# Performance work log

Measured on AMD Instinct MI355X. Metric: run time of the kernel, lower is better.

Reference implementation:

```python
import jax, jax.numpy as jnp
import numpy as np
import math

B, L, D, H, FF = 4, 1024, 1024, 16, 4096
DH = D // H
EPS = 1e-12


def layer_norm(x, gamma, beta):
    mean = x.mean(-1, keepdims=True)
    var = ((x - mean) ** 2).mean(-1, keepdims=True)  # biased var, matches unbiased=False
    return gamma * (x - mean) / jnp.sqrt(var + EPS) + beta


def setup_inputs() -> dict:
    key = jax.random.key(0)
    ks = jax.random.split(key, 16)
    s = 0.02
    return {
        "x": jax.random.normal(ks[0], (B, L, D), jnp.float32),
        "attn_bias": jax.random.uniform(ks[1], (B, L, L), jnp.float32),
        "src_mask": jax.random.randint(ks[2], (B, L), 0, 2, jnp.int32),
        "wq": jax.random.normal(ks[3], (D, D), jnp.float32) * s,
        "bq": jnp.zeros((D,), jnp.float32),
        "wk": jax.random.normal(ks[4], (D, D), jnp.float32) * s,
        "bk": jnp.zeros((D,), jnp.float32),
        "wv": jax.random.normal(ks[5], (D, D), jnp.float32) * s,
        "bv": jnp.zeros((D,), jnp.float32),
        "wo": jax.random.normal(ks[6], (D, D), jnp.float32) * s,
        "bo": jnp.zeros((D,), jnp.float32),
        "gamma1": jnp.ones((D,), jnp.float32),
        "beta1": jnp.zeros((D,), jnp.float32),
        "w1": jax.random.normal(ks[7], (D, FF), jnp.float32) * s,
        "b1": jnp.zeros((FF,), jnp.float32),
        "w2": jax.random.normal(ks[8], (FF, D), jnp.float32) * s,
        "b2": jnp.zeros((D,), jnp.float32),
        "gamma2": jnp.ones((D,), jnp.float32),
        "beta2": jnp.zeros((D,), jnp.float32),
    }


def reference(x, attn_bias, src_mask, wq, bq, wk, bk, wv, bv, wo, bo,
              gamma1, beta1, w1, b1, w2, b2, gamma2, beta2):
    # ---- multi-head attention with multiplicative bias + additive mask ----
    def split_heads(t):  # [B,L,D] -> [B,H,L,DH]
        return t.reshape(B, L, H, DH).transpose(0, 2, 1, 3)

    q = split_heads(x @ wq + bq)
    k = split_heads(x @ wk + bk)
    v = split_heads(x @ wv + bv)

    score = jnp.einsum('bhqd,bhkd->bhqk', q, k) / math.sqrt(DH)
    score = score * attn_bias[:, None, :, :]               # multiplicative bias
    score = jnp.where(src_mask[:, None, None, :] == 0, -10000.0, score)
    p = jax.nn.softmax(score, axis=-1)
    ctx = jnp.einsum('bhqk,bhkd->bhqd', p, v)
    ctx = ctx.transpose(0, 2, 1, 3).reshape(B, L, D)
    attn_out = ctx @ wo + bo

    h = layer_norm(x + attn_out, gamma1, beta1)

    # ---- position-wise FFN ----
    ffn = jax.nn.relu(h @ w1 + b1) @ w2 + b2
    out = layer_norm(h + ffn, gamma2, beta2)
    return out
```

## Files before the change

### kernel.cpp

```cpp
#include <hip/hip_runtime.h>
#include <hip/hip_bf16.h>
#include <math.h>

#define BB 4
#define LL 1024
#define DD 1024
#define HH 16
#define DHH 64
#define FFF 4096
#define MM (BB*LL)
#define LDQ 3072

typedef __attribute__((ext_vector_type(8))) short short8;
typedef __attribute__((ext_vector_type(4))) float f32x4;

__device__ __forceinline__ ushort f2bf(float f) {
    __hip_bfloat16 h = __float2bfloat16(f);
    return *(ushort*)&h;
}
__device__ __forceinline__ float bf2f(ushort u) {
    __hip_bfloat16 h = *(__hip_bfloat16*)&u;
    return __bfloat162float(h);
}
__device__ __forceinline__ float fexp2(float x) {
#if __has_builtin(__builtin_amdgcn_exp2f)
    return __builtin_amdgcn_exp2f(x);
#else
    return exp2f(x);
#endif
}

__device__ __forceinline__ float block_reduce_sum(float v, float* red, int tid) {
    red[tid] = v;
    __syncthreads();
    for (int off = 128; off > 0; off >>= 1) {
        if (tid < off) red[tid] += red[tid + off];
        __syncthreads();
    }
    float r = red[0];
    __syncthreads();
    return r;
}

__global__ __launch_bounds__(256)
void cast_bf16(const float* __restrict__ in, ushort* __restrict__ out) {
    const int i = blockIdx.x * 256 + threadIdx.x;
    float4 v = ((const float4*)in)[i];
    ushort4 o;
    o.x = f2bf(v.x); o.y = f2bf(v.y); o.z = f2bf(v.z); o.w = f2bf(v.w);
    ((ushort4*)out)[i] = o;
}

__global__ __launch_bounds__(256)
void swizzle_bias(const float* __restrict__ bias, float* __restrict__ B) {
    __shared__ float rowbuf[1024];
    const int row = blockIdx.x;
    const int t = threadIdx.x;
    *(float4*)&rowbuf[t * 4] = *(const float4*)&bias[(size_t)row * 1024 + t * 4];
    __syncthreads();
    const int kt = t >> 4, c = t & 15;
    const float s = 1.4426950408889634f;
    float4 o;
    o.x = rowbuf[kt * 64 + 0 * 16 + c] * s;
    o.y = rowbuf[kt * 64 + 1 * 16 + c] * s;
    o.z = rowbuf[kt * 64 + 2 * 16 + c] * s;
    o.w = rowbuf[kt * 64 + 3 * 16 + c] * s;
    *(float4*)&B[(size_t)row * 1024 + t * 4] = o;
}

__global__ __launch_bounds__(256)
void transpose_cast(const float* __restrict__ W, ushort* __restrict__ WT,
                    int K, int N) {
    __shared__ float tile[32][33];
    const int n0 = blockIdx.x * 32, k0 = blockIdx.y * 32;
    const int t = threadIdx.x;
    const int r = t >> 3, c4 = (t & 7) * 4;
    float4 v = *(const float4*)&W[(size_t)(k0 + r) * N + n0 + c4];
    tile[r][c4 + 0] = v.x; tile[r][c4 + 1] = v.y;
    tile[r][c4 + 2] = v.z; tile[r][c4 + 3] = v.w;
    __syncthreads();
    ushort4 o;
    o.x = f2bf(tile[c4 + 0][r]);
    o.y = f2bf(tile[c4 + 1][r]);
    o.z = f2bf(tile[c4 + 2][r]);
    o.w = f2bf(tile[c4 + 3][r]);
    *(ushort4*)&WT[(size_t)(n0 + r) * K + k0 + c4] = o;
}

__global__ __launch_bounds__(256)
void concat3(const float* __restrict__ a, const float* __restrict__ b,
             const float* __restrict__ c, float* __restrict__ o) {
    const int i = blockIdx.x * 256 + threadIdx.x;
    o[i] = (i < 1024) ? a[i] : ((i < 2048) ? b[i - 1024] : c[i - 2048]);
}

template<int BN>
__global__ __launch_bounds__(256)
void gemm_bf16(const ushort* __restrict__ A, const ushort* __restrict__ Bt,
               const float* __restrict__ bias, void* __restrict__ C,
               ushort* __restrict__ Vt, int vn0,
               int M, int N, int K, int relu, int obf16, int qlim) {
    constexpr int JF = BN / 32;
    __shared__ ushort Als0[128 * 32];
    __shared__ ushort Als1[128 * 32];
    __shared__ ushort Bls0[BN * 32];
    __shared__ ushort Bls1[BN * 32];

    const int L = blockIdx.x + gridDim.x * blockIdx.y;
    const int xcd = L & 7;
    const int idx = L >> 3;
    const int mpx = gridDim.y >> 3;
    const int bm = (xcd * mpx + (idx % mpx)) * 128;
    const int bn = (idx / mpx) * BN;

    const int t = threadIdx.x;
    const int lane = t & 63;
    const int w = t >> 6;
    const int wm = (w >> 1) * 64;
    const int wn = (w & 1) * (BN / 2);
    const int fm = lane & 15;
    const int kg = lane >> 4;

    f32x4 acc[4][JF] = {};

    for (int k0 = 0; k0 < K; k0 += 64) {
        #pragma unroll
        for (int j = 0; j < 2; ++j) {
            const int chunk = j * 256 + t;
            const int row = chunk >> 2, kc = chunk & 3;
            const ushort* ga0 = A + (size_t)(bm + row) * K + k0 + kc * 8;
            __builtin_amdgcn_global_load_lds(
                (const __attribute__((address_space(1))) void*)ga0,
                (__attribute__((address_space(3))) void*)(Als0 + chunk * 8), 16, 0, 0);
            const ushort* ga1 = ga0 + 32;
            __builtin_amdgcn_global_load_lds(
                (const __attribute__((address_space(1))) void*)ga1,
                (__attribute__((address_space(3))) void*)(Als1 + chunk * 8), 16, 0, 0);
        }
        #pragma unroll
        for (int j = 0; j < BN / 64; ++j) {
            const int chunk = j * 256 + t;
            const int row = chunk >> 2, kc = chunk & 3;
            const ushort* gb0 = Bt + (size_t)(bn + row) * K + k0 + kc * 8;
            __builtin_amdgcn_global_load_lds(
                (const __attribute__((address_space(1))) void*)gb0,
                (__attribute__((address_space(3))) void*)(Bls0 + chunk * 8), 16, 0, 0);
            const ushort* gb1 = gb0 + 32;
            __builtin_amdgcn_global_load_lds(
                (const __attribute__((address_space(1))) void*)gb1,
                (__attribute__((address_space(3))) void*)(Bls1 + chunk * 8), 16, 0, 0);
        }
        __syncthreads();

        short8 af[4][2], bfr[JF][2];
        #pragma unroll
        for (int i = 0; i < 4; ++i) {
            af[i][0] = *(const short8*)&Als0[(wm + i * 16 + fm) * 32 + kg * 8];
            af[i][1] = *(const short8*)&Als1[(wm + i * 16 + fm) * 32 + kg * 8];
        }
        #pragma unroll
        for (int j = 0; j < JF; ++j) {
            bfr[j][0] = *(const short8*)&Bls0[(wn + j * 16 + fm) * 32 + kg * 8];
            bfr[j][1] = *(const short8*)&Bls1[(wn + j * 16 + fm) * 32 + kg * 8];
        }
        #pragma unroll
        for (int i = 0; i < 4; ++i)
            #pragma unroll
            for (int j = 0; j < JF; ++j) {
                acc[i][j] = __builtin_amdgcn_mfma_f32_16x16x32_bf16(
                    af[i][0], bfr[j][0], acc[i][j], 0, 0, 0);
                acc[i][j] = __builtin_amdgcn_mfma_f32_16x16x32_bf16(
                    af[i][1], bfr[j][1], acc[i][j], 0, 0, 0);
            }
        __syncthreads();
    }

    const int orow0 = (lane >> 4) * 4;
    const int ocol = lane & 15;
    #pragma unroll
    for (int j = 0; j < JF; ++j) {
        const int n = bn + wn + j * 16 + ocol;
        const float bv = bias[n];
        const bool isV = (bn + wn + j * 16) >= vn0;
        #pragma unroll
        for (int i = 0; i < 4; ++i) {
            const int m0 = bm + wm + i * 16 + orow0;
            if (isV) {
                ushort4 o;
                float v0 = acc[i][j][0] + bv, v1 = acc[i][j][1] + bv;
                float v2 = acc[i][j][2] + bv, v3 = acc[i][j][3] + bv;
                o.x = f2bf(v0); o.y = f2bf(v1); o.z = f2bf(v2); o.w = f2bf(v3);
                *(ushort4*)&Vt[((size_t)((m0 >> 10) << 10) + (n - vn0)) * 1024 + (m0 & 1023)] = o;
            } else {
                #pragma unroll
                for (int r = 0; r < 4; ++r) {
                    const int m = m0 + r;
                    float v = acc[i][j][r] + bv;
                    if (relu) v = fmaxf(v, 0.0f);
                    if (n < qlim) v *= 0.125f;
                    if (obf16)
                        ((ushort*)C)[(size_t)m * N + n] = f2bf(v);
                    else
                        ((float*)C)[(size_t)m * N + n] = v;
                }
            }
        }
    }
}

template<int BN>
__global__ __launch_bounds__(256)
void gemm_bf16_sk(const ushort* __restrict__ A, const ushort* __restrict__ Bt,
                  float* __restrict__ P, int M, int N, int K) {
    constexpr int JF = BN / 32;
    __shared__ ushort Als0[128 * 32];
    __shared__ ushort Als1[128 * 32];
    __shared__ ushort Bls0[BN * 32];
    __shared__ ushort Bls1[BN * 32];

    const int L = blockIdx.x + gridDim.x * blockIdx.y;
    const int xcd = L & 7;
    const int idx = L >> 3;
    const int mpx = gridDim.y >> 3;
    const int bm = (xcd * mpx + (idx % mpx)) * 128;
    const int bn = (idx / mpx) * BN;
    const int kbeg = blockIdx.z * (K >> 1);
    const int kend = kbeg + (K >> 1);

    const int t = threadIdx.x;
    const int lane = t & 63;
    const int w = t >> 6;
    const int wm = (w >> 1) * 64;
    const int wn = (w & 1) * (BN / 2);
    const int fm = lane & 15;
    const int kg = lane >> 4;

    f32x4 acc[4][JF] = {};

    for (int k0 = kbeg; k0 < kend; k0 += 64) {
        #pragma unroll
        for (int j = 0; j < 2; ++j) {
            const int chunk = j * 256 + t;
            const int row = chunk >> 2, kc = chunk & 3;
            const ushort* ga0 = A + (size_t)(bm + row) * K + k0 + kc * 8;
            __builtin_amdgcn_global_load_lds(
                (const __attribute__((address_space(1))) void*)ga0,
                (__attribute__((address_space(3))) void*)(Als0 + chunk * 8), 16, 0, 0);
            const ushort* ga1 = ga0 + 32;
            __builtin_amdgcn_global_load_lds(
                (const __attribute__((address_space(1))) void*)ga1,
                (__attribute__((address_space(3))) void*)(Als1 + chunk * 8), 16, 0, 0);
        }
        #pragma unroll
        for (int j = 0; j < BN / 64; ++j) {
            const int chunk = j * 256 + t;
            const int row = chunk >> 2, kc = chunk & 3;
            const ushort* gb0 = Bt + (size_t)(bn + row) * K + k0 + kc * 8;
            __builtin_amdgcn_global_load_lds(
                (const __attribute__((address_space(1))) void*)gb0,
                (__attribute__((address_space(3))) void*)(Bls0 + chunk * 8), 16, 0, 0);
            const ushort* gb1 = gb0 + 32;
            __builtin_amdgcn_global_load_lds(
                (const __attribute__((address_space(1))) void*)gb1,
                (__attribute__((address_space(3))) void*)(Bls1 + chunk * 8), 16, 0, 0);
        }
        __syncthreads();

        short8 af[4][2], bfr[JF][2];
        #pragma unroll
        for (int i = 0; i < 4; ++i) {
            af[i][0] = *(const short8*)&Als0[(wm + i * 16 + fm) * 32 + kg * 8];
            af[i][1] = *(const short8*)&Als1[(wm + i * 16 + fm) * 32 + kg * 8];
        }
        #pragma unroll
        for (int j = 0; j < JF; ++j) {
            bfr[j][0] = *(const short8*)&Bls0[(wn + j * 16 + fm) * 32 + kg * 8];
            bfr[j][1] = *(const short8*)&Bls1[(wn + j * 16 + fm) * 32 + kg * 8];
        }
        #pragma unroll
        for (int i = 0; i < 4; ++i)
            #pragma unroll
            for (int j = 0; j < JF; ++j) {
                acc[i][j] = __builtin_amdgcn_mfma_f32_16x16x32_bf16(
                    af[i][0], bfr[j][0], acc[i][j], 0, 0, 0);
                acc[i][j] = __builtin_amdgcn_mfma_f32_16x16x32_bf16(
                    af[i][1], bfr[j][1], acc[i][j], 0, 0, 0);
            }
        __syncthreads();
    }

    float* Pz = P + (size_t)blockIdx.z * M * N;
    const int orow0 = (lane >> 4) * 4;
    const int ocol = lane & 15;
    #pragma unroll
    for (int j = 0; j < JF; ++j) {
        const int n = bn + wn + j * 16 + ocol;
        #pragma unroll
        for (int i = 0; i < 4; ++i) {
            const int m0 = bm + wm + i * 16 + orow0;
            #pragma unroll
            for (int r = 0; r < 4; ++r)
                Pz[(size_t)(m0 + r) * N + n] = acc[i][j][r];
        }
    }
}


#define BARM() asm volatile("s_barrier" ::: "memory")
#define VMC4() asm volatile("s_waitcnt vmcnt(4)" ::: "memory")
#define LGK0() do { asm volatile("s_waitcnt lgkmcnt(0)" ::: "memory"); \
                    __builtin_amdgcn_sched_barrier(0); } while (0)

__device__ __forceinline__ short8 fragrd(const ushort* h, int row, int s, int kg) {
    const int cb = ((s << 6) + (kg << 4)) ^ (((row >> 2) & 1) << 5);
    return *(const short8*)(h + row * 64 + (cb >> 1));
}

__device__ __forceinline__ void stage_half(const ushort* __restrict__ src,
                                           int srcK, ushort* ldsh, int t) {
    #pragma unroll
    for (int l = 0; l < 2; ++l) {
        const int chunk = l * 512 + t;
        const int r = chunk >> 3;
        const int cb_log = ((chunk & 7) * 16) ^ (((r >> 2) & 1) << 5);
        const ushort* g = src + (size_t)r * srcK + (cb_log >> 1);
        __builtin_amdgcn_global_load_lds(
            (const __attribute__((address_space(1))) void*)g,
            (__attribute__((address_space(3))) void*)(ldsh + chunk * 8), 16, 0, 0);
    }
}

__global__ __launch_bounds__(512, 2)
void gemm256(const ushort* __restrict__ A, const ushort* __restrict__ Bt,
             const float* __restrict__ bias, ushort* __restrict__ C,
             int M, int N, int K, int relu) {
    __shared__ ushort lds[65536];

    const int nt = K >> 6;
    const int t = threadIdx.x;
    const int lane = t & 63;
    const int w = t >> 6;
    const int wr = w >> 2, wc = w & 3;
    const int fm = lane & 15, kg = lane >> 4;

    const int bid = blockIdx.x;
    const int wg = (bid & 7) * (gridDim.x >> 3) + (bid >> 3);
    const int bm = (wg & 15) << 8;
    const int bn = (wg >> 4) << 8;

    ushort* const A0 = lds;
    ushort* const B0 = lds + 16384;
    ushort* const A1 = lds + 32768;
    ushort* const B1 = lds + 49152;

    const ushort* const Ah0 = A0 + wr * 8192;
    const ushort* const Ah1 = A1 + wr * 8192;
    const ushort* const Bh0 = B0 + (wc >> 1) * 8192;
    const ushort* const Bh1 = B1 + (wc >> 1) * 8192;
    const int brow = (wc & 1) * 64;

    #define ASRC(tt, h) (A  + (size_t)(bm + (h) * 128) * K + (tt) * 64)
    #define BSRC(tt, h) (Bt + (size_t)(bn + (h) * 128) * K + (tt) * 64)

    f32x4 acc[8][4] = {};
    short8 af[4][2];
    short8 bf2[4][2];

    #define RD_A(HP, MI0) do { \
        _Pragma("unroll") \
        for (int i = 0; i < 4; ++i) { \
            const int row = ((MI0) + i) * 16 + fm; \
            af[i][0] = fragrd((HP), row, 0, kg); \
            af[i][1] = fragrd((HP), row, 1, kg); \
        } } while (0)

    #define RD_B(HP, J0) do { \
        _Pragma("unroll") \
        for (int jj = 0; jj < 2; ++jj) { \
            const int row = brow + ((J0) + jj) * 16 + fm; \
            bf2[(J0) + jj][0] = fragrd((HP), row, 0, kg); \
            bf2[(J0) + jj][1] = fragrd((HP), row, 1, kg); \
        } } while (0)

    #define QMFMA(MI0, J0) do { \
        __builtin_amdgcn_s_setprio(1); \
        _Pragma("unroll") \
        for (int i = 0; i < 4; ++i) { \
            _Pragma("unroll") \
            for (int jj = 0; jj < 2; ++jj) { \
                acc[(MI0)+i][(J0)+jj] = __builtin_amdgcn_mfma_f32_16x16x32_bf16( \
                    af[i][0], bf2[(J0)+jj][0], acc[(MI0)+i][(J0)+jj], 0, 0, 0); \
                acc[(MI0)+i][(J0)+jj] = __builtin_amdgcn_mfma_f32_16x16x32_bf16( \
                    af[i][1], bf2[(J0)+jj][1], acc[(MI0)+i][(J0)+jj], 0, 0, 0); \
            } } \
        __builtin_amdgcn_s_setprio(0); \
    } while (0)

    stage_half(BSRC(0, 0), K, B0, t);
    stage_half(BSRC(0, 1), K, B0 + 8192, t);
    stage_half(ASRC(0, 0), K, A0, t);
    stage_half(ASRC(0, 1), K, A0 + 8192, t);
    stage_half(BSRC(1, 0), K, B1, t);
    stage_half(BSRC(1, 1), K, B1 + 8192, t);
    VMC4();
    BARM();

    for (int it = 0; it < (nt >> 1); ++it) {
        const int ta = 2 * it;
        const int tb = ta + 1;
        const int t2 = min(ta + 2, nt - 1);
        const int t3 = min(ta + 3, nt - 1);

        RD_A(Ah0, 0); RD_B(Bh0, 0);
        stage_half(ASRC(tb, 0), K, A1, t);
        BARM(); LGK0(); QMFMA(0, 0); BARM();
        RD_B(Bh0, 2);
        stage_half(ASRC(tb, 1), K, A1 + 8192, t);
        BARM(); LGK0(); QMFMA(0, 2); BARM();
        RD_A(Ah0, 4);
        stage_half(BSRC(t2, 0), K, B0, t);
        BARM(); LGK0(); QMFMA(4, 2); BARM();
        stage_half(BSRC(t2, 1), K, B0 + 8192, t);
        VMC4();
        BARM(); LGK0(); QMFMA(4, 0); BARM();
        RD_A(Ah1, 0); RD_B(Bh1, 0);
        stage_half(ASRC(t2, 0), K, A0, t);
        BARM(); LGK0(); QMFMA(0, 0); BARM();
        RD_B(Bh1, 2);
        stage_half(ASRC(t2, 1), K, A0 + 8192, t);
        BARM(); LGK0(); QMFMA(0, 2); BARM();
        RD_A(Ah1, 4);
        stage_half(BSRC(t3, 0), K, B1, t);
        BARM(); LGK0(); QMFMA(4, 2); BARM();
        stage_half(BSRC(t3, 1), K, B1 + 8192, t);
        VMC4();
        BARM(); LGK0(); QMFMA(4, 0); BARM();
    }

    const int oc = lane & 15, og = lane >> 4;
    #pragma unroll
    for (int nj = 0; nj < 4; ++nj) {
        const int n = bn + wc * 64 + nj * 16 + oc;
        const float bv = bias[n];
        #pragma unroll
        for (int mi = 0; mi < 8; ++mi) {
            const int m0 = bm + wr * 128 + mi * 16 + og * 4;
            #pragma unroll
            for (int r = 0; r < 4; ++r) {
                float v = acc[mi][nj][r] + bv;
                if (relu) v = fmaxf(v, 0.0f);
                C[(size_t)(m0 + r) * N + n] = f2bf(v);
            }
        }
    }
    #undef ASRC
    #undef BSRC
    #undef RD_A
    #undef RD_B
    #undef QMFMA
}

__global__ __launch_bounds__(256, 4)
void attn_mfma(const ushort* __restrict__ QKVb, const ushort* __restrict__ Vt,
               const float* __restrict__ biasw, const int* __restrict__ mask,
               ushort* __restrict__ ctx) {
    const int q0 = blockIdx.x * 64;
    const int h = blockIdx.y;
    const int b = blockIdx.z;
    const int t = threadIdx.x;
    const int lane = t & 63;
    const int w = t >> 6;
    const int g = lane >> 4;
    const int c = lane & 15;

    __shared__ ushort QP[64 * 72];
    __shared__ ushort Ks[64 * 72];
    __shared__ ushort Vs[64 * 72];
    __shared__ float maskS[LL];

    #pragma unroll
    for (int i = 0; i < 2; ++i) {
        const int chunk = i * 256 + t;
        const int row = chunk >> 3, c8 = (chunk & 7) * 8;
        *(short8*)&QP[row * 72 + c8] =
            *(const short8*)(QKVb + ((size_t)(b * LL + q0 + row)) * LDQ + h * DHH + c8);
    }
    {
        int4 mi = ((const int4*)(mask + b * LL))[t];
        float4 mf;
        mf.x = mi.x ? 0.0f : -49152.0f;
        mf.y = mi.y ? 0.0f : -49152.0f;
        mf.z = mi.z ? 0.0f : -49152.0f;
        mf.w = mi.w ? 0.0f : -49152.0f;
        ((float4*)maskS)[t] = mf;
    }

    short8 pk[2], pv[2];
    #pragma unroll
    for (int i = 0; i < 2; ++i) {
        const int chunk = i * 256 + t;
        const int row = chunk >> 3, c8 = (chunk & 7) * 8;
        pk[i] = *(const short8*)(QKVb + ((size_t)(b * LL + row)) * LDQ + 1024 + h * DHH + c8);
        pv[i] = *(const short8*)(Vt + ((size_t)((b * HH + h) * DHH + row)) * LL + c8);
    }
    __syncthreads();

    short8 aq0 = *(const short8*)&QP[(w * 16 + c) * 72 + g * 8];
    short8 aq1 = *(const short8*)&QP[(w * 16 + c) * 72 + g * 8 + 32];
    ushort* Pw = QP + w * (16 * 72);

    const float* bp = biasw + (size_t)(b * LL + q0 + w * 16 + 4 * g) * 1024 + c * 4;
    float4 pb[4];
    #pragma unroll
    for (int r = 0; r < 4; ++r)
        pb[r] = *(const float4*)(bp + r * 1024);

    float l_run[4] = {0.f, 0.f, 0.f, 0.f};
    f32x4 acc_o[4] = {};

    for (int kt = 0; kt < 16; ++kt) {
        #pragma unroll
        for (int i = 0; i < 2; ++i) {
            const int chunk = i * 256 + t;
            const int row = chunk >> 3, c8 = (chunk & 7) * 8;
            *(short8*)&Ks[row * 72 + c8] = pk[i];
            *(short8*)&Vs[row * 72 + c8] = pv[i];
        }
        __syncthreads();

        if (kt < 15) {
            const int k0n = (kt + 1) * 64;
            #pragma unroll
            for (int i = 0; i < 2; ++i) {
                const int chunk = i * 256 + t;
                const int row = chunk >> 3, c8 = (chunk & 7) * 8;
                pk[i] = *(const short8*)(QKVb + ((size_t)(b * LL + k0n + row)) * LDQ + 1024 + h * DHH + c8);
                pv[i] = *(const short8*)(Vt + ((size_t)((b * HH + h) * DHH + row)) * LL + k0n + c8);
            }
        }

        float4 pbn[4];
        if (kt < 15) {
            #pragma unroll
            for (int r = 0; r < 4; ++r)
                pbn[r] = *(const float4*)(bp + r * 1024 + (kt + 1) * 64);
        }

        float mk[4];
        #pragma unroll
        for (int j = 0; j < 4; ++j) mk[j] = maskS[kt * 64 + j * 16 + c];

        f32x4 accs[4] = {};
        __builtin_amdgcn_s_setprio(1);
        #pragma unroll
        for (int j = 0; j < 4; ++j) {
            short8 bk0 = *(const short8*)&Ks[(j * 16 + c) * 72 + g * 8];
            short8 bk1 = *(const short8*)&Ks[(j * 16 + c) * 72 + g * 8 + 32];
            accs[j] = __builtin_amdgcn_mfma_f32_16x16x32_bf16(aq0, bk0, accs[j], 0, 0, 0);
            accs[j] = __builtin_amdgcn_mfma_f32_16x16x32_bf16(aq1, bk1, accs[j], 0, 0, 0);
        }
        __builtin_amdgcn_s_setprio(0);

        #pragma unroll
        for (int j = 0; j < 4; ++j)
            #pragma unroll
            for (int r = 0; r < 4; ++r) {
                const float pe = fexp2(fmaf(accs[j][r], ((const float*)&pb[r])[j], mk[j]));
                l_run[r] += pe;
                Pw[(4 * g + r) * 72 + j * 16 + c] = f2bf(pe);
            }

        __builtin_amdgcn_s_setprio(1);
        #pragma unroll
        for (int ks = 0; ks < 2; ++ks) {
            short8 ap = *(const short8*)&Pw[c * 72 + ks * 32 + g * 8];
            #pragma unroll
            for (int j = 0; j < 4; ++j) {
                short8 bv8 = *(const short8*)&Vs[(j * 16 + c) * 72 + ks * 32 + g * 8];
                acc_o[j] = __builtin_amdgcn_mfma_f32_16x16x32_bf16(ap, bv8, acc_o[j], 0, 0, 0);
            }
        }
        __builtin_amdgcn_s_setprio(0);

        if (kt < 15) {
            #pragma unroll
            for (int r = 0; r < 4; ++r) pb[r] = pbn[r];
        }
        __syncthreads();
    }

    #pragma unroll
    for (int r = 0; r < 4; ++r) {
        float l = l_run[r];
        #pragma unroll
        for (int d = 1; d < 16; d <<= 1) l += __shfl_xor(l, d);
        const float inv = 1.0f / l;
        #pragma unroll
        for (int j = 0; j < 4; ++j)
            ctx[((size_t)(b * LL + q0 + w * 16 + 4 * g + r)) * DD + h * DHH + j * 16 + c] =
                f2bf(acc_o[j][r] * inv);
    }
}

__global__ __launch_bounds__(256)
void add_ln_kernel(const float* __restrict__ P0, const float* __restrict__ P1,
                   const float* __restrict__ cb, const float* __restrict__ bres,
                   const float* __restrict__ gamma, const float* __restrict__ beta,
                   float* __restrict__ out, ushort* __restrict__ outb) {
    const int row = blockIdx.x;
    const int tid = threadIdx.x;
    __shared__ float red[256];

    const size_t base = (size_t)row * DD;
    float v[4];
    float sum = 0.0f;
    #pragma unroll
    for (int i = 0; i < 4; ++i) {
        const int col = tid + i * 256;
        v[i] = P0[base + col] + P1[base + col] + cb[col] + bres[base + col];
        sum += v[i];
    }
    const float mean = block_reduce_sum(sum, red, tid) * (1.0f / 1024.0f);
    float vs = 0.0f;
    #pragma unroll
    for (int i = 0; i < 4; ++i) {
        const float dlt = v[i] - mean;
        vs += dlt * dlt;
    }
    const float var = block_reduce_sum(vs, red, tid) * (1.0f / 1024.0f);
    const float rstd = rsqrtf(var + 1e-12f);
    #pragma unroll
    for (int i = 0; i < 4; ++i) {
        const int col = tid + i * 256;
        const float o = gamma[col] * (v[i] - mean) * rstd + beta[col];
        out[base + col] = o;
        if (outb) outb[base + col] = f2bf(o);
    }
}

extern "C" void kernel_launch(void* const* d_in, const int* in_sizes, int n_in,
                              void* d_out, int out_size, void* d_ws, size_t ws_size,
                              hipStream_t stream) {
    const float* x         = (const float*)d_in[0];
    const float* attn_bias = (const float*)d_in[1];
    const int*   src_mask  = (const int*)  d_in[2];
    const float* wq = (const float*)d_in[3];
    const float* bq = (const float*)d_in[4];
    const float* wk = (const float*)d_in[5];
    const float* bk = (const float*)d_in[6];
    const float* wv = (const float*)d_in[7];
    const float* bv = (const float*)d_in[8];
    const float* wo = (const float*)d_in[9];
    const float* bo = (const float*)d_in[10];
    const float* gamma1 = (const float*)d_in[11];
    const float* beta1  = (const float*)d_in[12];
    const float* w1 = (const float*)d_in[13];
    const float* b1 = (const float*)d_in[14];
    const float* w2 = (const float*)d_in[15];
    const float* b2 = (const float*)d_in[16];
    const float* gamma2 = (const float*)d_in[17];
    const float* beta2  = (const float*)d_in[18];
    float* out = (float*)d_out;

    const size_t MB = 1024 * 1024;
    char* W = (char*)d_ws;
    ushort* xb    = (ushort*)(W + 0);
    ushort* ctxb  = (ushort*)(W + 0);
    ushort* W1T   = (ushort*)(W + 0);
    ushort* QKVb  = (ushort*)(W + 8 * MB);
    float*  Hb    = (float*) (W + 8 * MB);
    ushort* Hbb   = (ushort*)(W + 24 * MB);
    ushort* W2T   = (ushort*)(W + 24 * MB);
    ushort* F1b   = (ushort*)(W + 32 * MB);
    ushort* Vt    = (ushort*)(W + 40 * MB);
    ushort* WQKVT = (ushort*)(W + 48 * MB);
    ushort* WOT   = (ushort*)(W + 48 * MB);
    float*  bqkv  = (float*) (W + 62 * MB);
    float*  biasw = (float*) (W + 64 * MB);
    float*  P0    = (float*) (W + 64 * MB);

    dim3 blk(256);

    cast_bf16<<<dim3(4096), blk, 0, stream>>>(x, xb);
    swizzle_bias<<<dim3(4096), blk, 0, stream>>>(attn_bias, biasw);
    transpose_cast<<<dim3(32, 32), blk, 0, stream>>>(wq, WQKVT, DD, DD);
    transpose_cast<<<dim3(32, 32), blk, 0, stream>>>(wk, WQKVT + 1024 * 1024, DD, DD);
    transpose_cast<<<dim3(32, 32), blk, 0, stream>>>(wv, WQKVT + 2048 * 1024, DD, DD);
    concat3<<<dim3(12), blk, 0, stream>>>(bq, bk, bv, bqkv);
    gemm_bf16<128><<<dim3(24, 32), blk, 0, stream>>>(xb, WQKVT, bqkv, QKVb,
                                                     Vt, 2048, MM, LDQ, DD, 0, 1, 1024);
    attn_mfma<<<dim3(16, HH, BB), blk, 0, stream>>>(QKVb, Vt, biasw, src_mask, ctxb);
    transpose_cast<<<dim3(32, 32), blk, 0, stream>>>(wo, WOT, DD, DD);
    gemm_bf16_sk<64><<<dim3(16, 32, 2), blk, 0, stream>>>(ctxb, WOT, P0, MM, DD, DD);
    transpose_cast<<<dim3(128, 32), blk, 0, stream>>>(w1, W1T, DD, FFF);
    add_ln_kernel<<<dim3(MM), blk, 0, stream>>>(P0, P0 + (size_t)MM * DD, bo, x,
                                                gamma1, beta1, Hb, Hbb);
    gemm256<<<dim3(256), dim3(512), 0, stream>>>(Hbb, W1T, b1, F1b, MM, FFF, DD, 1);
    transpose_cast<<<dim3(32, 128), blk, 0, stream>>>(w2, W2T, FFF, DD);
    gemm_bf16_sk<64><<<dim3(16, 32, 2), blk, 0, stream>>>(F1b, W2T, P0, MM, DD, FFF);
    add_ln_kernel<<<dim3(MM), blk, 0, stream>>>(P0, P0 + (size_t)MM * DD, b2, Hb,
                                                gamma2, beta2, out, nullptr);
}
```

Baseline: 374.6 us.

## Run QKV projection through 256x256 gemm256 kernel and widen LDS swizzle

The fused QKV projection now uses the larger 256x256-tile gemm256 kernel instead of the 128x128 gemm_bf16, which is removed. gemm256's epilogue gains the V-transpose write and Q scaling so it can produce the QKV outputs. The LDS XOR swizzle changes from a single-bit pattern to an eight-way (row & 7) pattern to cut bank conflicts on fragment reads. The larger tiles raise data reuse but launch only 192 workgroups, which may leave some compute units idle.

```diff
diff --git a/kernel.cpp b/kernel.cpp
--- a/kernel.cpp
+++ b/kernel.cpp
@@ -96,10 +96,8 @@
 
 template<int BN>
 __global__ __launch_bounds__(256)
-void gemm_bf16(const ushort* __restrict__ A, const ushort* __restrict__ Bt,
-               const float* __restrict__ bias, void* __restrict__ C,
-               ushort* __restrict__ Vt, int vn0,
-               int M, int N, int K, int relu, int obf16, int qlim) {
+void gemm_bf16_sk(const ushort* __restrict__ A, const ushort* __restrict__ Bt,
+                  float* __restrict__ P, int M, int N, int K) {
     constexpr int JF = BN / 32;
     __shared__ ushort Als0[128 * 32];
     __shared__ ushort Als1[128 * 32];
@@ -112,6 +110,8 @@
     const int mpx = gridDim.y >> 3;
     const int bm = (xcd * mpx + (idx % mpx)) * 128;
     const int bn = (idx / mpx) * BN;
+    const int kbeg = blockIdx.z * (K >> 1);
+    const int kend = kbeg + (K >> 1);
 
     const int t = threadIdx.x;
     const int lane = t & 63;
@@ -123,7 +123,7 @@
 
     f32x4 acc[4][JF] = {};
 
-    for (int k0 = 0; k0 < K; k0 += 64) {
+    for (int k0 = kbeg; k0 < kend; k0 += 64) {
         #pragma unroll
         for (int j = 0; j < 2; ++j) {
             const int chunk = j * 256 + t;
@@ -175,120 +175,6 @@
         __syncthreads();
     }
 
-    const int orow0 = (lane >> 4) * 4;
-    const int ocol = lane & 15;
-    #pragma unroll
-    for (int j = 0; j < JF; ++j) {
-        const int n = bn + wn + j * 16 + ocol;
-        const float bv = bias[n];
-        const bool isV = (bn + wn + j * 16) >= vn0;
-        #pragma unroll
-        for (int i = 0; i < 4; ++i) {
-            const int m0 = bm + wm + i * 16 + orow0;
-            if (isV) {
-                ushort4 o;
-                float v0 = acc[i][j][0] + bv, v1 = acc[i][j][1] + bv;
-                float v2 = acc[i][j][2] + bv, v3 = acc[i][j][3] + bv;
-                o.x = f2bf(v0); o.y = f2bf(v1); o.z = f2bf(v2); o.w = f2bf(v3);
-                *(ushort4*)&Vt[((size_t)((m0 >> 10) << 10) + (n - vn0)) * 1024 + (m0 & 1023)] = o;
-            } else {
-                #pragma unroll
-                for (int r = 0; r < 4; ++r) {
-                    const int m = m0 + r;
-                    float v = acc[i][j][r] + bv;
-                    if (relu) v = fmaxf(v, 0.0f);
-                    if (n < qlim) v *= 0.125f;
-                    if (obf16)
-                        ((ushort*)C)[(size_t)m * N + n] = f2bf(v);
-                    else
-                        ((float*)C)[(size_t)m * N + n] = v;
-                }
-            }
-        }
-    }
-}
-
-template<int BN>
-__global__ __launch_bounds__(256)
-void gemm_bf16_sk(const ushort* __restrict__ A, const ushort* __restrict__ Bt,
-                  float* __restrict__ P, int M, int N, int K) {
-    constexpr int JF = BN / 32;
-    __shared__ ushort Als0[128 * 32];
-    __shared__ ushort Als1[128 * 32];
-    __shared__ ushort Bls0[BN * 32];
-    __shared__ ushort Bls1[BN * 32];
-
-    const int L = blockIdx.x + gridDim.x * blockIdx.y;
-    const int xcd = L & 7;
-    const int idx = L >> 3;
-    const int mpx = gridDim.y >> 3;
-    const int bm = (xcd * mpx + (idx % mpx)) * 128;
-    const int bn = (idx / mpx) * BN;
-    const int kbeg = blockIdx.z * (K >> 1);
-    const int kend = kbeg + (K >> 1);
-
-    const int t = threadIdx.x;
-    const int lane = t & 63;
-    const int w = t >> 6;
-    const int wm = (w >> 1) * 64;
-    const int wn = (w & 1) * (BN / 2);
-    const int fm = lane & 15;
-    const int kg = lane >> 4;
-
-    f32x4 acc[4][JF] = {};
-
-    for (int k0 = kbeg; k0 < kend; k0 += 64) {
-        #pragma unroll
-        for (int j = 0; j < 2; ++j) {
-            const int chunk = j * 256 + t;
-            const int row = chunk >> 2, kc = chunk & 3;
-            const ushort* ga0 = A + (size_t)(bm + row) * K + k0 + kc * 8;
-            __builtin_amdgcn_global_load_lds(
-                (const __attribute__((address_space(1))) void*)ga0,
-                (__attribute__((address_space(3))) void*)(Als0 + chunk * 8), 16, 0, 0);
-            const ushort* ga1 = ga0 + 32;
-            __builtin_amdgcn_global_load_lds(
-                (const __attribute__((address_space(1))) void*)ga1,
-                (__attribute__((address_space(3))) void*)(Als1 + chunk * 8), 16, 0, 0);
-        }
-        #pragma unroll
-        for (int j = 0; j < BN / 64; ++j) {
-            const int chunk = j * 256 + t;
-            const int row = chunk >> 2, kc = chunk & 3;
-            const ushort* gb0 = Bt + (size_t)(bn + row) * K + k0 + kc * 8;
-            __builtin_amdgcn_global_load_lds(
-                (const __attribute__((address_space(1))) void*)gb0,
-                (__attribute__((address_space(3))) void*)(Bls0 + chunk * 8), 16, 0, 0);
-            const ushort* gb1 = gb0 + 32;
-            __builtin_amdgcn_global_load_lds(
-                (const __attribute__((address_space(1))) void*)gb1,
-                (__attribute__((address_space(3))) void*)(Bls1 + chunk * 8), 16, 0, 0);
-        }
-        __syncthreads();
-
-        short8 af[4][2], bfr[JF][2];
-        #pragma unroll
-        for (int i = 0; i < 4; ++i) {
-            af[i][0] = *(const short8*)&Als0[(wm + i * 16 + fm) * 32 + kg * 8];
-            af[i][1] = *(const short8*)&Als1[(wm + i * 16 + fm) * 32 + kg * 8];
-        }
-        #pragma unroll
-        for (int j = 0; j < JF; ++j) {
-            bfr[j][0] = *(const short8*)&Bls0[(wn + j * 16 + fm) * 32 + kg * 8];
-            bfr[j][1] = *(const short8*)&Bls1[(wn + j * 16 + fm) * 32 + kg * 8];
-        }
-        #pragma unroll
-        for (int i = 0; i < 4; ++i)
-            #pragma unroll
-            for (int j = 0; j < JF; ++j) {
-                acc[i][j] = __builtin_amdgcn_mfma_f32_16x16x32_bf16(
-                    af[i][0], bfr[j][0], acc[i][j], 0, 0, 0);
-                acc[i][j] = __builtin_amdgcn_mfma_f32_16x16x32_bf16(
-                    af[i][1], bfr[j][1], acc[i][j], 0, 0, 0);
-            }
-        __syncthreads();
-    }
-
     float* Pz = P + (size_t)blockIdx.z * M * N;
     const int orow0 = (lane >> 4) * 4;
     const int ocol = lane & 15;
@@ -312,7 +198,7 @@
                     __builtin_amdgcn_sched_barrier(0); } while (0)
 
 __device__ __forceinline__ short8 fragrd(const ushort* h, int row, int s, int kg) {
-    const int cb = ((s << 6) + (kg << 4)) ^ (((row >> 2) & 1) << 5);
+    const int cb = ((s << 6) + (kg << 4)) ^ ((row & 7) << 4);
     return *(const short8*)(h + row * 64 + (cb >> 1));
 }
 
@@ -322,7 +208,7 @@
     for (int l = 0; l < 2; ++l) {
         const int chunk = l * 512 + t;
         const int r = chunk >> 3;
-        const int cb_log = ((chunk & 7) * 16) ^ (((r >> 2) & 1) << 5);
+        const int cb_log = ((chunk & 7) * 16) ^ ((r & 7) << 4);
         const ushort* g = src + (size_t)r * srcK + (cb_log >> 1);
         __builtin_amdgcn_global_load_lds(
             (const __attribute__((address_space(1))) void*)g,
@@ -333,7 +219,8 @@
 __global__ __launch_bounds__(512, 2)
 void gemm256(const ushort* __restrict__ A, const ushort* __restrict__ Bt,
              const float* __restrict__ bias, ushort* __restrict__ C,
-             int M, int N, int K, int relu) {
+             ushort* __restrict__ Vt, int vn0,
+             int M, int N, int K, int relu, int qlim) {
     __shared__ ushort lds[65536];
 
     const int nt = K >> 6;
@@ -440,16 +327,28 @@
     const int oc = lane & 15, og = lane >> 4;
     #pragma unroll
     for (int nj = 0; nj < 4; ++nj) {
-        const int n = bn + wc * 64 + nj * 16 + oc;
+        const int nb = bn + wc * 64 + nj * 16;
+        const int n = nb + oc;
         const float bv = bias[n];
+        const bool isV = nb >= vn0;
         #pragma unroll
         for (int mi = 0; mi < 8; ++mi) {
             const int m0 = bm + wr * 128 + mi * 16 + og * 4;
-            #pragma unroll
-            for (int r = 0; r < 4; ++r) {
-                float v = acc[mi][nj][r] + bv;
-                if (relu) v = fmaxf(v, 0.0f);
-                C[(size_t)(m0 + r) * N + n] = f2bf(v);
+            if (isV) {
+                ushort4 o;
+                o.x = f2bf(acc[mi][nj][0] + bv);
+                o.y = f2bf(acc[mi][nj][1] + bv);
+                o.z = f2bf(acc[mi][nj][2] + bv);
+                o.w = f2bf(acc[mi][nj][3] + bv);
+                *(ushort4*)&Vt[((size_t)((m0 >> 10) << 10) + (n - vn0)) * 1024 + (m0 & 1023)] = o;
+            } else {
+                #pragma unroll
+                for (int r = 0; r < 4; ++r) {
+                    float v = acc[mi][nj][r] + bv;
+                    if (relu) v = fmaxf(v, 0.0f);
+                    if (n < qlim) v *= 0.125f;
+                    C[(size_t)(m0 + r) * N + n] = f2bf(v);
+                }
             }
         }
     }
@@ -687,15 +586,16 @@
     transpose_cast<<<dim3(32, 32), blk, 0, stream>>>(wk, WQKVT + 1024 * 1024, DD, DD);
     transpose_cast<<<dim3(32, 32), blk, 0, stream>>>(wv, WQKVT + 2048 * 1024, DD, DD);
     concat3<<<dim3(12), blk, 0, stream>>>(bq, bk, bv, bqkv);
-    gemm_bf16<128><<<dim3(24, 32), blk, 0, stream>>>(xb, WQKVT, bqkv, QKVb,
-                                                     Vt, 2048, MM, LDQ, DD, 0, 1, 1024);
+    gemm256<<<dim3(192), dim3(512), 0, stream>>>(xb, WQKVT, bqkv, QKVb,
+                                                 Vt, 2048, MM, LDQ, DD, 0, 1024);
     attn_mfma<<<dim3(16, HH, BB), blk, 0, stream>>>(QKVb, Vt, biasw, src_mask, ctxb);
     transpose_cast<<<dim3(32, 32), blk, 0, stream>>>(wo, WOT, DD, DD);
     gemm_bf16_sk<64><<<dim3(16, 32, 2), blk, 0, stream>>>(ctxb, WOT, P0, MM, DD, DD);
     transpose_cast<<<dim3(128, 32), blk, 0, stream>>>(w1, W1T, DD, FFF);
     add_ln_kernel<<<dim3(MM), blk, 0, stream>>>(P0, P0 + (size_t)MM * DD, bo, x,
                                                 gamma1, beta1, Hb, Hbb);
-    gemm256<<<dim3(256), dim3(512), 0, stream>>>(Hbb, W1T, b1, F1b, MM, FFF, DD, 1);
+    gemm256<<<dim3(256), dim3(512), 0, stream>>>(Hbb, W1T, b1, F1b,
+                                                 Vt, 1 << 30, MM, FFF, DD, 1, 0);
     transpose_cast<<<dim3(32, 128), blk, 0, stream>>>(w2, W2T, FFF, DD);
     gemm_bf16_sk<64><<<dim3(16, 32, 2), blk, 0, stream>>>(F1b, W2T, P0, MM, DD, FFF);
     add_ln_kernel<<<dim3(MM), blk, 0, stream>>>(P0, P0 + (size_t)MM * DD, b2, Hb,
```

Result: slower. 386.7 us (+3.2%).
